# Kernel tuning notes

Hardware: AMD Instinct MI355X
Metric: run time of the kernel (lower is better)

Reference implementation:

```python
import jax, jax.numpy as jnp
import numpy as np
from jax import lax

B, S, V, U = 32, 512, 8000, 1024  # batch, seq_len, vocab, enc_units


def setup_inputs() -> dict:
    key = jax.random.key(0)
    ks = jax.random.split(key, 9)

    def p(k, shape, s=0.05):
        return jax.random.normal(k, shape, dtype=jnp.float32) * s

    inp = {"tokens": jax.random.randint(ks[0], (B, S), 0, V)}
    i = 1
    for d in ("f", "b"):  # forward / backward directions
        inp[f"W1{d}"] = p(ks[i], (V, 3 * U)); i += 1      # layer-1 input kernel (acts on one-hot)
        inp[f"R1{d}"] = p(ks[i], (U, 3 * U)); i += 1      # layer-1 recurrent kernel
        inp[f"b1{d}"] = jnp.zeros((2, 3 * U), jnp.float32)  # [input_bias, recurrent_bias] (reset_after)
        inp[f"W2{d}"] = p(ks[i], (U, 3 * U)); i += 1      # layer-2 input kernel
        inp[f"R2{d}"] = p(ks[i], (U, 3 * U)); i += 1
        inp[f"b2{d}"] = jnp.zeros((2, 3 * U), jnp.float32)
    return inp


def _gru_step(xz, h, R, rb):
    # Keras GRUCell, reset_after=True, inference (recurrent_dropout inactive).
    zi, ri, hi = jnp.split(xz, 3, axis=-1)
    rz, rr, rh = jnp.split(h @ R + rb, 3, axis=-1)
    z = jax.nn.sigmoid(zi + rz)
    r = jax.nn.sigmoid(ri + rr)
    hh = jnp.tanh(hi + r * rh)
    return z * h + (1.0 - z) * hh


def _run_dir(tokens, W1, R1, b1, W2, R2, b2, reverse):
    # one_hot(tokens) @ W1 == row gather of W1 (same math, no [B,S,V] one-hot materialized)
    x1 = jnp.take(W1, tokens, axis=0) + b1[0]  # [B, S, 3U]
    if reverse:
        x1 = x1[:, ::-1]
    units = R1.shape[0]
    h0 = jnp.zeros((tokens.shape[0], units), x1.dtype)

    def step(carry, xt):
        h1, h2 = carry
        h1 = _gru_step(xt, h1, R1, b1[1])
        h2 = _gru_step(h1 @ W2 + b2[0], h2, R2, b2[1])
        return (h1, h2), h2

    (h1, h2), ys = lax.scan(step, (h0, h0), jnp.swapaxes(x1, 0, 1))
    ys = jnp.swapaxes(ys, 0, 1)  # [B, S, U]
    if reverse:
        ys = ys[:, ::-1]
    return ys, h1, h2


def reference(tokens, W1f, R1f, b1f, W2f, R2f, b2f, W1b, R1b, b1b, W2b, R2b, b2b):
    yf, hf1, hf2 = _run_dir(tokens, W1f, R1f, b1f, W2f, R2f, b2f, False)
    yb, hb1, hb2 = _run_dir(tokens, W1b, R1b, b1b, W2b, R2b, b2b, True)
    output = jnp.concatenate([yf, yb], axis=-1)  # Bidirectional merge_mode='concat' -> [B,S,2U]
    # Faithful to the module's state indexing: s = [fwd_l1, fwd_l2, bwd_l1, bwd_l2];
    # getBidirectionalStates concatenates s[2i], s[2i+1].
    state1 = jnp.concatenate([hf1, hf2], axis=-1)
    state2 = jnp.concatenate([hb1, hb2], axis=-1)
    return output, state1, state2
```

## Files before the change

kernel.cpp:

```cpp
#include <hip/hip_runtime.h>
#include <stdint.h>

typedef __bf16 bf16x8 __attribute__((ext_vector_type(8)));
typedef float  f32x4  __attribute__((ext_vector_type(4)));

#define YSZ 33554432ull

#define R1L_OFF 0ull
#define R2L_OFF 12582912ull
#define W2L_OFF 25165824ull
#define HR1_OFF 37748736ull
#define HR2_OFF 39845888ull
#define X2R_OFF 41943040ull
#define FLG_OFF 48234496ull
#define WS_NEED 48238592ull

#define SM_RECW 0
#define SM_XW0  98304
#define SM_XW1  131072
#define SM_RED0 147456
#define SM_RED1 150528
#define SM_HST  153600
#define SM_XST  154624
#define SM_BYTES 156160

__device__ __forceinline__ unsigned short f2bf(float x){
  unsigned u; __builtin_memcpy(&u, &x, 4);
  u = (u + 0x7fffu + ((u >> 16) & 1u)) >> 16;
  return (unsigned short)u;
}
__device__ __forceinline__ float bf2f(unsigned short s){
  unsigned u = ((unsigned)s) << 16; float f; __builtin_memcpy(&f, &u, 4); return f;
}
__device__ __forceinline__ f32x4 mfma16(bf16x8 a, bf16x8 b, f32x4 c){
  return __builtin_amdgcn_mfma_f32_16x16x32_bf16(a, b, c, 0, 0, 0);
}

__global__ __launch_bounds__(256) void prep_weights(
    const float* __restrict__ R1f, const float* __restrict__ W2f, const float* __restrict__ R2f,
    const float* __restrict__ R1b, const float* __restrict__ W2b, const float* __restrict__ R2b,
    unsigned short* __restrict__ dst)
{
  unsigned c = blockIdx.x * 256u + threadIdx.x;
  if (c >= 2359296u) return;
  unsigned reg, cc;
  if (c < 786432u)       { reg = 0; cc = c; }
  else if (c < 1572864u) { reg = 1; cc = c - 786432u; }
  else                   { reg = 2; cc = c - 1572864u; }
  unsigned dirq = cc / 393216u; unsigned r = cc % 393216u;
  const float* src; unsigned col, ktbase, kg4;
  if (reg < 2) {
    unsigned a = r / 6144u; r %= 6144u;
    unsigned g = r / 2048u; r %= 2048u;
    unsigned kt = r >> 6;  unsigned l = r & 63u;
    col = g*1024u + a*16u + (l & 15u);
    ktbase = kt*32u; kg4 = (l >> 4)*4u;
    src = (reg==0) ? (dirq ? R1b : R1f) : (dirq ? R2b : R2f);
  } else {
    unsigned s = r / 3072u; unsigned rr = r % 3072u;
    unsigned c0 = s * 24u;
    if (rr < 2048u) { unsigned kt = rr >> 6, l = rr & 63u; col = c0 + (l & 15u); ktbase = kt*32u; kg4 = (l>>4)*4u; }
    else { unsigned q = rr - 2048u; unsigned kt = q >> 5, sl = q & 31u; col = c0 + 16u + (sl & 7u); ktbase = kt*32u; kg4 = (sl >> 3)*4u; }
    src = dirq ? W2b : W2f;
  }
  unsigned short* d = dst + (size_t)c * 8u;
  #pragma unroll
  for (int j = 0; j < 8; ++j) {
    unsigned k = ktbase + ((j >> 2) << 4) + kg4 + (j & 3);
    d[j] = f2bf(src[(size_t)k * 3072u + col]);
  }
}

__device__ __forceinline__ void poll_ge(unsigned* base, int lane, int tgt, long* budget){
  if (tgt <= 0 || *budget <= 0) return;
  long it = 0;
  while (1) {
    unsigned v = __hip_atomic_load(base + lane, __ATOMIC_RELAXED, __HIP_MEMORY_SCOPE_AGENT);
    if (__all((int)v >= tgt)) return;
    if (++it > *budget) { *budget = 0; return; }
    __builtin_amdgcn_s_sleep(1);
  }
}
__device__ __forceinline__ bf16x8 ld_frag(const char* slot, int kt, int mt, int lane){
  const uint64_t* p = (const uint64_t*)(slot + (((size_t)(kt*2 + mt)*64 + lane) << 4));
  union { uint64_t u[2]; bf16x8 v; } f;
  f.u[0] = __hip_atomic_load((uint64_t*)p,     __ATOMIC_RELAXED, __HIP_MEMORY_SCOPE_AGENT);
  f.u[1] = __hip_atomic_load((uint64_t*)p + 1, __ATOMIC_RELAXED, __HIP_MEMORY_SCOPE_AGENT);
  return f.v;
}
__device__ __forceinline__ void st16c(char* dst, const char* srcLDS){
  const uint64_t* s = (const uint64_t*)srcLDS;
  uint64_t a = s[0], b = s[1];
  __hip_atomic_store((uint64_t*)dst,     a, __ATOMIC_RELAXED, __HIP_MEMORY_SCOPE_AGENT);
  __hip_atomic_store((uint64_t*)dst + 1, b, __ATOMIC_RELAXED, __HIP_MEMORY_SCOPE_AGENT);
}

__global__ __launch_bounds__(256, 1) void enc_main(
    const int* __restrict__ tokens,
    const float* __restrict__ W1f, const float* __restrict__ W1b,
    const float* __restrict__ b1f, const float* __restrict__ b1b,
    const float* __restrict__ b2f, const float* __restrict__ b2b,
    char* __restrict__ ws, float* __restrict__ out)
{
  extern __shared__ char smem[];
  const int tid  = threadIdx.x;
  const int lane = tid & 63;
  const int wave = tid >> 6;
  const int mt   = wave >> 1;
  const int kh   = wave & 1;
  const int bid  = blockIdx.x;
  const int role = bid >> 6;
  const int idx  = bid & 63;
  const int dir  = role >> 1;
  const int isC  = role & 1;
  const int u0   = idx * 16;
  const int kt0  = u0 >> 5;
  const int uh8  = ((u0 >> 4) & 1) * 8;
  const int i16  = lane & 15;
  const int lg   = lane >> 4;

  {
    const size_t recoff = (isC ? R2L_OFF : R1L_OFF) + (size_t)(dir*64 + idx) * 98304;
    const uint4* rs = (const uint4*)(ws + recoff);
    uint4* rd = (uint4*)(smem + SM_RECW);
    #pragma unroll
    for (int i = 0; i < 24; ++i) rd[tid + 256*i] = rs[tid + 256*i];
    const size_t xoff = W2L_OFF + (size_t)(dir*128 + (isC ? 64 : 0) + idx) * 49152;
    const uint4* xs = (const uint4*)(ws + xoff);
    uint4* xd = (uint4*)(smem + SM_XW0);
    #pragma unroll
    for (int i = 0; i < 12; ++i) xd[tid + 256*i] = xs[tid + 256*i];
  }
  __syncthreads();

  unsigned* flags = (unsigned*)(ws + FLG_OFF);
  unsigned* fA1 = flags +   0 + dir*64;
  unsigned* fA2 = flags + 128 + dir*64;
  unsigned* fC1 = flags + 256 + dir*64;
  unsigned* fC2 = flags + 384 + dir*64;
  char* hr1 = ws + HR1_OFF + (size_t)dir * 16 * 65536;
  char* hr2 = ws + HR2_OFF + (size_t)dir * 16 * 65536;
  char* x2r = ws + X2R_OFF + (size_t)dir * 16 * 196608;
  const float* W1 = dir ? W1b : W1f;
  const float* b1 = dir ? b1b : b1f;
  const float* b2 = dir ? b2b : b2f;

  union FZ { uint64_t u[2]; bf16x8 v; };
  FZ fz; fz.u[0] = 0; fz.u[1] = 0;
  const bf16x8 zfrag = fz.v;

  long budget = 4000000;

  if (!isC) {
    const int c0x = idx * 24;
    bf16x8 hfr[16];
    #pragma unroll
    for (int q = 0; q < 16; ++q) hfr[q] = zfrag;
    float hold[4] = {0.f, 0.f, 0.f, 0.f};
    float x1z[4], x1r[4], x1h[4];
    float b0z=0,b0r=0,b0h=0,brz=0,brr=0,brh=0;
    if (kh == 0) {
      b0z = b1[u0 + i16]; b0r = b1[1024 + u0 + i16]; b0h = b1[2048 + u0 + i16];
      brz = b1[3072 + u0 + i16]; brr = b1[4096 + u0 + i16]; brh = b1[5120 + u0 + i16];
      int tt = dir ? 511 : 0;
      #pragma unroll
      for (int r = 0; r < 4; ++r) {
        int m = mt*16 + lg*4 + r;
        int tok = tokens[m*512 + tt];
        const float* p = W1 + (size_t)tok*3072 + u0 + i16;
        x1z[r] = p[0]; x1r[r] = p[1024]; x1h[r] = p[2048];
      }
    }
    for (int t = 0; t < 512; ++t) {
      float nz[4], nr[4], nh[4];
      if (kh == 0 && t < 511) {
        int tt = dir ? (510 - t) : (t + 1);
        #pragma unroll
        for (int r = 0; r < 4; ++r) {
          int m = mt*16 + lg*4 + r;
          int tok = tokens[m*512 + tt];
          const float* p = W1 + (size_t)tok*3072 + u0 + i16;
          nz[r] = p[0]; nr[r] = p[1024]; nh[r] = p[2048];
        }
      }
      f32x4 az = {0,0,0,0}, ar = {0,0,0,0}, ah = {0,0,0,0};
      #pragma unroll
      for (int q = 0; q < 16; ++q) {
        int kt = kh*16 + q;
        bf16x8 a = hfr[q];
        az = mfma16(a, *(const bf16x8*)(smem + SM_RECW +         (kt<<10) + (lane<<4)), az);
        ar = mfma16(a, *(const bf16x8*)(smem + SM_RECW + 32768 + (kt<<10) + (lane<<4)), ar);
        ah = mfma16(a, *(const bf16x8*)(smem + SM_RECW + 65536 + (kt<<10) + (lane<<4)), ah);
      }
      __syncthreads();
      if (kh == 1) {
        f32x4* red = (f32x4*)(smem + (mt ? SM_RED1 : SM_RED0));
        red[lane] = az; red[64 + lane] = ar; red[128 + lane] = ah;
      }
      __syncthreads();
      if (kh == 0) {
        const f32x4* red = (const f32x4*)(smem + (mt ? SM_RED1 : SM_RED0));
        f32x4 rz = red[lane], rr4 = red[64 + lane], rh = red[128 + lane];
        #pragma unroll
        for (int r = 0; r < 4; ++r) {
          float zp = x1z[r] + b0z + az[r] + rz[r] + brz;
          float rp = x1r[r] + b0r + ar[r] + rr4[r] + brr;
          float zg = 1.f / (1.f + __expf(-zp));
          float rg = 1.f / (1.f + __expf(-rp));
          float hp = (x1h[r] + b0h) + rg * (ah[r] + rh[r] + brh);
          float e2 = __expf(-2.f * hp);
          float th = (1.f - e2) / (1.f + e2);
          float hn = zg * hold[r] + (1.f - zg) * th;
          hold[r] = hn;
          *(unsigned short*)(smem + SM_HST + ((mt*16 + lg*4 + r)*16 + i16)*2) = f2bf(hn);
        }
        if (t == 511) {
          #pragma unroll
          for (int r = 0; r < 4; ++r)
            out[YSZ + (size_t)dir*65536 + (size_t)(mt*16 + lg*4 + r)*2048 + u0 + i16] = hold[r];
        }
      }
      __syncthreads();
      char* h1slot = hr1 + (size_t)(t & 15) * 65536;
      if (wave == 0) {
        poll_ge(fC1, lane, t - 15, &budget);
        #pragma unroll
        for (int mtl = 0; mtl < 2; ++mtl) {
          uint64_t v = *(const uint64_t*)(smem + SM_HST + (mtl*256 + (lane & 15)*16 + ((lane >> 4) << 2))*2);
          __hip_atomic_store((uint64_t*)(h1slot + (((size_t)(kt0*2 + mtl)*64 + lane) << 4) + uh8),
                             v, __ATOMIC_RELAXED, __HIP_MEMORY_SCOPE_AGENT);
        }
        if (lane == 0)
          __hip_atomic_store(fA1 + idx, (unsigned)(t + 1), __ATOMIC_RELEASE, __HIP_MEMORY_SCOPE_AGENT);
        poll_ge(fA1, lane, t + 1, &budget);
      }
      __syncthreads();
      #pragma unroll
      for (int q = 0; q < 16; ++q) hfr[q] = ld_frag(h1slot, kh*16 + q, mt, lane);
      f32x4 a0 = {0,0,0,0}, a1 = {0,0,0,0};
      #pragma unroll
      for (int q = 0; q < 16; ++q) {
        int kt = kh*16 + q;
        bf16x8 a = hfr[q];
        a0 = mfma16(a, *(const bf16x8*)(smem + SM_XW0 + (kt<<10) + (lane<<4)), a0);
        bf16x8 bb = zfrag;
        if (i16 < 8) bb = *(const bf16x8*)(smem + SM_XW1 + (kt<<9) + ((lg*8 + (lane & 7)) << 4));
        a1 = mfma16(a, bb, a1);
      }
      __syncthreads();
      if (kh == 1) {
        f32x4* red = (f32x4*)(smem + (mt ? SM_RED1 : SM_RED0));
        red[lane] = a0; red[64 + lane] = a1;
      }
      __syncthreads();
      if (kh == 0) {
        const f32x4* red = (const f32x4*)(smem + (mt ? SM_RED1 : SM_RED0));
        f32x4 r0 = red[lane], r1 = red[64 + lane];
        #pragma unroll
        for (int r = 0; r < 4; ++r) {
          int m = mt*16 + lg*4 + r;
          *(unsigned short*)(smem + SM_XST + (i16*32 + m)*2) = f2bf(a0[r] + r0[r]);
          if (i16 < 8)
            *(unsigned short*)(smem + SM_XST + ((16 + i16)*32 + m)*2) = f2bf(a1[r] + r1[r]);
        }
      }
      __syncthreads();
      if (wave == 0) {
        char* xslot = x2r + (size_t)(t & 15) * 196608;
        st16c(xslot + (size_t)(c0x + (lane >> 2))*64 + (lane & 3)*16,
              smem + SM_XST + (lane >> 2)*64 + (lane & 3)*16);
        if (lane < 32) {
          int c = 64 + lane;
          st16c(xslot + (size_t)(c0x + (c >> 2))*64 + (c & 3)*16,
                smem + SM_XST + (c >> 2)*64 + (c & 3)*16);
        }
        if (lane == 0)
          __hip_atomic_store(fA2 + idx, (unsigned)(t + 1), __ATOMIC_RELEASE, __HIP_MEMORY_SCOPE_AGENT);
      }
      if (kh == 0 && t < 511) {
        #pragma unroll
        for (int r = 0; r < 4; ++r) { x1z[r] = nz[r]; x1r[r] = nr[r]; x1h[r] = nh[r]; }
      }
    }
  } else {
    const int c0x = 1536 + idx * 24;
    bf16x8 hf2[16], hf1[16];
    #pragma unroll
    for (int q = 0; q < 16; ++q) { hf2[q] = zfrag; hf1[q] = zfrag; }
    float hold[4] = {0.f, 0.f, 0.f, 0.f};
    float b0z=0,b0r=0,b0h=0,brz=0,brr=0,brh=0;
    if (kh == 0) {
      b0z = b2[u0 + i16]; b0r = b2[1024 + u0 + i16]; b0h = b2[2048 + u0 + i16];
      brz = b2[3072 + u0 + i16]; brr = b2[4096 + u0 + i16]; brh = b2[5120 + u0 + i16];
    }
    for (int t = 0; t < 512; ++t) {
      if (wave == 0 && t > 0) poll_ge(fC1, lane, t, &budget);
      __syncthreads();
      if (t > 0) {
        char* h2slot = hr2 + (size_t)((t - 1) & 15) * 65536;
        #pragma unroll
        for (int q = 0; q < 16; ++q) hf2[q] = ld_frag(h2slot, kh*16 + q, mt, lane);
      }
      f32x4 az = {0,0,0,0}, ar = {0,0,0,0}, ah = {0,0,0,0};
      #pragma unroll
      for (int q = 0; q < 16; ++q) {
        int kt = kh*16 + q;
        bf16x8 a = hf2[q];
        az = mfma16(a, *(const bf16x8*)(smem + SM_RECW +         (kt<<10) + (lane<<4)), az);
        ar = mfma16(a, *(const bf16x8*)(smem + SM_RECW + 32768 + (kt<<10) + (lane<<4)), ar);
        ah = mfma16(a, *(const bf16x8*)(smem + SM_RECW + 65536 + (kt<<10) + (lane<<4)), ah);
      }
      __syncthreads();
      if (kh == 1) {
        f32x4* red = (f32x4*)(smem + (mt ? SM_RED1 : SM_RED0));
        red[lane] = az; red[64 + lane] = ar; red[128 + lane] = ah;
      }
      __syncthreads();
      f32x4 rz = {0,0,0,0}, rr4 = {0,0,0,0}, rh = {0,0,0,0};
      if (kh == 0) {
        const f32x4* red = (const f32x4*)(smem + (mt ? SM_RED1 : SM_RED0));
        rz = red[lane]; rr4 = red[64 + lane]; rh = red[128 + lane];
      }
      if (wave == 0) poll_ge(fA1, lane, t + 1, &budget);
      __syncthreads();
      char* h1slot = hr1 + (size_t)(t & 15) * 65536;
      #pragma unroll
      for (int q = 0; q < 16; ++q) hf1[q] = ld_frag(h1slot, kh*16 + q, mt, lane);
      f32x4 a0 = {0,0,0,0}, a1 = {0,0,0,0};
      #pragma unroll
      for (int q = 0; q < 16; ++q) {
        int kt = kh*16 + q;
        bf16x8 a = hf1[q];
        a0 = mfma16(a, *(const bf16x8*)(smem + SM_XW0 + (kt<<10) + (lane<<4)), a0);
        bf16x8 bb = zfrag;
        if (i16 < 8) bb = *(const bf16x8*)(smem + SM_XW1 + (kt<<9) + ((lg*8 + (lane & 7)) << 4));
        a1 = mfma16(a, bb, a1);
      }
      __syncthreads();
      if (kh == 1) {
        f32x4* red = (f32x4*)(smem + (mt ? SM_RED1 : SM_RED0));
        red[lane] = a0; red[64 + lane] = a1;
      }
      __syncthreads();
      if (kh == 0) {
        const f32x4* red = (const f32x4*)(smem + (mt ? SM_RED1 : SM_RED0));
        f32x4 r0 = red[lane], r1 = red[64 + lane];
        #pragma unroll
        for (int r = 0; r < 4; ++r) {
          int m = mt*16 + lg*4 + r;
          *(unsigned short*)(smem + SM_XST + (i16*32 + m)*2) = f2bf(a0[r] + r0[r]);
          if (i16 < 8)
            *(unsigned short*)(smem + SM_XST + ((16 + i16)*32 + m)*2) = f2bf(a1[r] + r1[r]);
        }
      }
      __syncthreads();
      char* xslot = x2r + (size_t)(t & 15) * 196608;
      if (wave == 0) {
        st16c(xslot + (size_t)(c0x + (lane >> 2))*64 + (lane & 3)*16,
              smem + SM_XST + (lane >> 2)*64 + (lane & 3)*16);
        if (lane < 32) {
          int c = 64 + lane;
          st16c(xslot + (size_t)(c0x + (c >> 2))*64 + (c & 3)*16,
                smem + SM_XST + (c >> 2)*64 + (c & 3)*16);
        }
        if (lane == 0)
          __hip_atomic_store(fC2 + idx, (unsigned)(t + 1), __ATOMIC_RELEASE, __HIP_MEMORY_SCOPE_AGENT);
        poll_ge(fA2, lane, t + 1, &budget);
        poll_ge(fC2, lane, t + 1, &budget);
      }
      __syncthreads();
      if (kh == 0) {
        int m0 = mt*16 + lg*4;
        float xg[3][4];
        #pragma unroll
        for (int g = 0; g < 3; ++g) {
          uint64_t v = __hip_atomic_load(
              (uint64_t*)(xslot + ((size_t)(g*1024 + u0 + i16)*32 + m0)*2),
              __ATOMIC_RELAXED, __HIP_MEMORY_SCOPE_AGENT);
          #pragma unroll
          for (int r = 0; r < 4; ++r) xg[g][r] = bf2f((unsigned short)(v >> (16*r)));
        }
        int tt = dir ? (511 - t) : t;
        #pragma unroll
        for (int r = 0; r < 4; ++r) {
          float zp = xg[0][r] + b0z + az[r] + rz[r] + brz;
          float rp = xg[1][r] + b0r + ar[r] + rr4[r] + brr;
          float zg = 1.f / (1.f + __expf(-zp));
          float rg = 1.f / (1.f + __expf(-rp));
          float hp = (xg[2][r] + b0h) + rg * (ah[r] + rh[r] + brh);
          float e2 = __expf(-2.f * hp);
          float th = (1.f - e2) / (1.f + e2);
          float hn = zg * hold[r] + (1.f - zg) * th;
          hold[r] = hn;
          *(unsigned short*)(smem + SM_HST + ((mt*16 + lg*4 + r)*16 + i16)*2) = f2bf(hn);
          int m = m0 + r;
          out[((size_t)m*512 + tt)*2048 + dir*1024 + u0 + i16] = hn;
          if (t == 511)
            out[YSZ + (size_t)dir*65536 + (size_t)m*2048 + 1024 + u0 + i16] = hn;
        }
      }
      __syncthreads();
      if (wave == 0) {
        char* h2slot = hr2 + (size_t)(t & 15) * 65536;
        #pragma unroll
        for (int mtl = 0; mtl < 2; ++mtl) {
          uint64_t v = *(const uint64_t*)(smem + SM_HST + (mtl*256 + (lane & 15)*16 + ((lane >> 4) << 2))*2);
          __hip_atomic_store((uint64_t*)(h2slot + (((size_t)(kt0*2 + mtl)*64 + lane) << 4) + uh8),
                             v, __ATOMIC_RELAXED, __HIP_MEMORY_SCOPE_AGENT);
        }
        if (lane == 0)
          __hip_atomic_store(fC1 + idx, (unsigned)(t + 1), __ATOMIC_RELEASE, __HIP_MEMORY_SCOPE_AGENT);
      }
    }
  }
}

extern "C" void kernel_launch(void* const* d_in, const int* in_sizes, int n_in,
                              void* d_out, int out_size, void* d_ws, size_t ws_size,
                              hipStream_t stream)
{
  const int*   tokens = (const int*)d_in[0];
  const float* W1f = (const float*)d_in[1];
  const float* R1f = (const float*)d_in[2];
  const float* b1f = (const float*)d_in[3];
  const float* W2f = (const float*)d_in[4];
  const float* R2f = (const float*)d_in[5];
  const float* b2f = (const float*)d_in[6];
  const float* W1b = (const float*)d_in[7];
  const float* R1b = (const float*)d_in[8];
  const float* b1b = (const float*)d_in[9];
  const float* W2b = (const float*)d_in[10];
  const float* R2b = (const float*)d_in[11];
  const float* b2b = (const float*)d_in[12];
  char* ws = (char*)d_ws;
  (void)in_sizes; (void)n_in; (void)out_size;
  if (ws_size < WS_NEED) return;

  hipMemsetAsync(ws + FLG_OFF, 0, 4096, stream);
  prep_weights<<<9216, 256, 0, stream>>>(R1f, W2f, R2f, R1b, W2b, R2b, (unsigned short*)ws);
  hipFuncSetAttribute((const void*)enc_main, hipFuncAttributeMaxDynamicSharedMemorySize, 163840);
  enc_main<<<256, 256, SM_BYTES, stream>>>(tokens, W1f, W1b, b1f, b1b, b2f, b2b, ws, (float*)d_out);
}
```

Before: 10.14 ms.

## Move layer-2 input projection into layer-2 blocks and drop x2 exchange buffer

```diff
diff --git a/kernel.cpp b/kernel.cpp
--- a/kernel.cpp
+++ b/kernel.cpp
@@ -11,58 +11,45 @@
 #define W2L_OFF 25165824ull
 #define HR1_OFF 37748736ull
 #define HR2_OFF 39845888ull
-#define X2R_OFF 41943040ull
-#define FLG_OFF 48234496ull
-#define WS_NEED 48238592ull
+#define FLG_OFF 41943040ull
+#define WS_NEED 41947136ull
 
 #define SM_RECW 0
-#define SM_XW0  98304
-#define SM_XW1  131072
-#define SM_RED0 147456
-#define SM_RED1 150528
-#define SM_HST  153600
-#define SM_XST  154624
-#define SM_BYTES 156160
+#define SM_XWH  98304
+#define SM_RED0 131072
+#define SM_RED1 135168
+#define SM_HST  139264
+#define SM_BYTES 140288
 
 __device__ __forceinline__ unsigned short f2bf(float x){
   unsigned u; __builtin_memcpy(&u, &x, 4);
   u = (u + 0x7fffu + ((u >> 16) & 1u)) >> 16;
   return (unsigned short)u;
 }
-__device__ __forceinline__ float bf2f(unsigned short s){
-  unsigned u = ((unsigned)s) << 16; float f; __builtin_memcpy(&f, &u, 4); return f;
-}
 __device__ __forceinline__ f32x4 mfma16(bf16x8 a, bf16x8 b, f32x4 c){
   return __builtin_amdgcn_mfma_f32_16x16x32_bf16(a, b, c, 0, 0, 0);
 }
 
 __global__ __launch_bounds__(256) void prep_weights(
-    const float* __restrict__ R1f, const float* __restrict__ W2f, const float* __restrict__ R2f,
-    const float* __restrict__ R1b, const float* __restrict__ W2b, const float* __restrict__ R2b,
+    const float* __restrict__ R1f, const float* __restrict__ R2f, const float* __restrict__ W2f,
+    const float* __restrict__ R1b, const float* __restrict__ R2b, const float* __restrict__ W2b,
     unsigned short* __restrict__ dst)
 {
   unsigned c = blockIdx.x * 256u + threadIdx.x;
   if (c >= 2359296u) return;
-  unsigned reg, cc;
-  if (c < 786432u)       { reg = 0; cc = c; }
-  else if (c < 1572864u) { reg = 1; cc = c - 786432u; }
-  else                   { reg = 2; cc = c - 1572864u; }
-  unsigned dirq = cc / 393216u; unsigned r = cc % 393216u;
-  const float* src; unsigned col, ktbase, kg4;
-  if (reg < 2) {
-    unsigned a = r / 6144u; r %= 6144u;
-    unsigned g = r / 2048u; r %= 2048u;
-    unsigned kt = r >> 6;  unsigned l = r & 63u;
-    col = g*1024u + a*16u + (l & 15u);
-    ktbase = kt*32u; kg4 = (l >> 4)*4u;
-    src = (reg==0) ? (dirq ? R1b : R1f) : (dirq ? R2b : R2f);
-  } else {
-    unsigned s = r / 3072u; unsigned rr = r % 3072u;
-    unsigned c0 = s * 24u;
-    if (rr < 2048u) { unsigned kt = rr >> 6, l = rr & 63u; col = c0 + (l & 15u); ktbase = kt*32u; kg4 = (l>>4)*4u; }
-    else { unsigned q = rr - 2048u; unsigned kt = q >> 5, sl = q & 31u; col = c0 + 16u + (sl & 7u); ktbase = kt*32u; kg4 = (sl >> 3)*4u; }
-    src = dirq ? W2b : W2f;
-  }
+  unsigned reg = c / 786432u;
+  unsigned cc  = c % 786432u;
+  unsigned dirq = cc / 393216u;
+  unsigned r = cc % 393216u;
+  unsigned a = r / 6144u; r %= 6144u;
+  unsigned g = r / 2048u; r %= 2048u;
+  unsigned kt = r >> 6; unsigned l = r & 63u;
+  unsigned col = g*1024u + a*16u + (l & 15u);
+  unsigned ktbase = kt*32u, kg4 = (l >> 4)*4u;
+  const float* src;
+  if (reg == 0)      src = dirq ? R1b : R1f;
+  else if (reg == 1) src = dirq ? R2b : R2f;
+  else               src = dirq ? W2b : W2f;
   unsigned short* d = dst + (size_t)c * 8u;
   #pragma unroll
   for (int j = 0; j < 8; ++j) {
@@ -71,11 +58,13 @@
   }
 }
 
-__device__ __forceinline__ void poll_ge(unsigned* base, int lane, int tgt, long* budget){
+__device__ __forceinline__ void poll_ge2(unsigned* base, int lane, int tgt, long* budget){
   if (tgt <= 0 || *budget <= 0) return;
   long it = 0;
   while (1) {
-    unsigned v = __hip_atomic_load(base + lane, __ATOMIC_RELAXED, __HIP_MEMORY_SCOPE_AGENT);
+    unsigned v0 = __hip_atomic_load(base + lane,      __ATOMIC_RELAXED, __HIP_MEMORY_SCOPE_AGENT);
+    unsigned v1 = __hip_atomic_load(base + 64 + lane, __ATOMIC_RELAXED, __HIP_MEMORY_SCOPE_AGENT);
+    unsigned v = v0 < v1 ? v0 : v1;
     if (__all((int)v >= tgt)) return;
     if (++it > *budget) { *budget = 0; return; }
     __builtin_amdgcn_s_sleep(1);
@@ -88,11 +77,11 @@
   f.u[1] = __hip_atomic_load((uint64_t*)p + 1, __ATOMIC_RELAXED, __HIP_MEMORY_SCOPE_AGENT);
   return f.v;
 }
-__device__ __forceinline__ void st16c(char* dst, const char* srcLDS){
-  const uint64_t* s = (const uint64_t*)srcLDS;
-  uint64_t a = s[0], b = s[1];
-  __hip_atomic_store((uint64_t*)dst,     a, __ATOMIC_RELAXED, __HIP_MEMORY_SCOPE_AGENT);
-  __hip_atomic_store((uint64_t*)dst + 1, b, __ATOMIC_RELAXED, __HIP_MEMORY_SCOPE_AGENT);
+__device__ __forceinline__ uint64_t lds_transpose_read(const char* p){
+  asm volatile("" ::: "memory");
+  __builtin_amdgcn_sched_barrier(0);
+  uint64_t v; __builtin_memcpy(&v, p, 8);
+  return v;
 }
 
 __global__ __launch_bounds__(256, 1) void enc_main(
@@ -119,44 +108,35 @@
   const int i16  = lane & 15;
   const int lg   = lane >> 4;
 
+  unsigned* flags = (unsigned*)(ws + FLG_OFF);
+  unsigned* fA1 = flags + dir*128;
+  unsigned* fC1 = flags + 256 + dir*128;
+  char* hr1 = ws + HR1_OFF + (size_t)dir * 1048576;
+  char* hr2 = ws + HR2_OFF + (size_t)dir * 1048576;
+  const float* b1 = dir ? b1b : b1f;
+  const float* b2 = dir ? b2b : b2f;
+  const float* W1 = dir ? W1b : W1f;
+
+  union FZ { uint64_t u[2]; bf16x8 v; };
+  FZ fz; fz.u[0] = 0; fz.u[1] = 0;
+  const bf16x8 zfrag = fz.v;
+
+  long budget = 2000000;
+
   {
     const size_t recoff = (isC ? R2L_OFF : R1L_OFF) + (size_t)(dir*64 + idx) * 98304;
     const uint4* rs = (const uint4*)(ws + recoff);
     uint4* rd = (uint4*)(smem + SM_RECW);
     #pragma unroll
     for (int i = 0; i < 24; ++i) rd[tid + 256*i] = rs[tid + 256*i];
-    const size_t xoff = W2L_OFF + (size_t)(dir*128 + (isC ? 64 : 0) + idx) * 49152;
-    const uint4* xs = (const uint4*)(ws + xoff);
-    uint4* xd = (uint4*)(smem + SM_XW0);
-    #pragma unroll
-    for (int i = 0; i < 12; ++i) xd[tid + 256*i] = xs[tid + 256*i];
   }
-  __syncthreads();
-
-  unsigned* flags = (unsigned*)(ws + FLG_OFF);
-  unsigned* fA1 = flags +   0 + dir*64;
-  unsigned* fA2 = flags + 128 + dir*64;
-  unsigned* fC1 = flags + 256 + dir*64;
-  unsigned* fC2 = flags + 384 + dir*64;
-  char* hr1 = ws + HR1_OFF + (size_t)dir * 16 * 65536;
-  char* hr2 = ws + HR2_OFF + (size_t)dir * 16 * 65536;
-  char* x2r = ws + X2R_OFF + (size_t)dir * 16 * 196608;
-  const float* W1 = dir ? W1b : W1f;
-  const float* b1 = dir ? b1b : b1f;
-  const float* b2 = dir ? b2b : b2f;
-
-  union FZ { uint64_t u[2]; bf16x8 v; };
-  FZ fz; fz.u[0] = 0; fz.u[1] = 0;
-  const bf16x8 zfrag = fz.v;
-
-  long budget = 4000000;
 
   if (!isC) {
-    const int c0x = idx * 24;
+    __syncthreads();
     bf16x8 hfr[16];
     #pragma unroll
     for (int q = 0; q < 16; ++q) hfr[q] = zfrag;
-    float hold[4] = {0.f, 0.f, 0.f, 0.f};
+    float hold[4] = {0.f,0.f,0.f,0.f};
     float x1z[4], x1r[4], x1h[4];
     float b0z=0,b0r=0,b0h=0,brz=0,brr=0,brh=0;
     if (kh == 0) {
@@ -198,6 +178,7 @@
         red[lane] = az; red[64 + lane] = ar; red[128 + lane] = ah;
       }
       __syncthreads();
+      char* h1slot = hr1 + (size_t)(t & 15) * 65536;
       if (kh == 0) {
         const f32x4* red = (const f32x4*)(smem + (mt ? SM_RED1 : SM_RED0));
         f32x4 rz = red[lane], rr4 = red[64 + lane], rh = red[128 + lane];
@@ -214,202 +195,112 @@
           hold[r] = hn;
           *(unsigned short*)(smem + SM_HST + ((mt*16 + lg*4 + r)*16 + i16)*2) = f2bf(hn);
         }
-        if (t == 511) {
+        uint64_t v = lds_transpose_read(smem + SM_HST + ((mt*16 + i16)*16 + lg*4)*2);
+        if ((t & 7) == 0) poll_ge2(fC1, lane, t - 7, &budget);
+        __hip_atomic_store((uint64_t*)(h1slot + (((size_t)(kt0*2 + mt)*64 + lane) << 4) + uh8),
+                           v, __ATOMIC_RELAXED, __HIP_MEMORY_SCOPE_AGENT);
+        if (lane == 0)
+          __hip_atomic_store(fA1 + mt*64 + idx, (unsigned)(t + 1), __ATOMIC_RELEASE, __HIP_MEMORY_SCOPE_AGENT);
+      }
+      if (t < 511) {
+        poll_ge2(fA1, lane, t + 1, &budget);
+        #pragma unroll
+        for (int q = 0; q < 16; ++q) hfr[q] = ld_frag(h1slot, kh*16 + q, mt, lane);
+        if (kh == 0) {
           #pragma unroll
-          for (int r = 0; r < 4; ++r)
-            out[YSZ + (size_t)dir*65536 + (size_t)(mt*16 + lg*4 + r)*2048 + u0 + i16] = hold[r];
-        }
-      }
-      __syncthreads();
-      char* h1slot = hr1 + (size_t)(t & 15) * 65536;
-      if (wave == 0) {
-        poll_ge(fC1, lane, t - 15, &budget);
-        #pragma unroll
-        for (int mtl = 0; mtl < 2; ++mtl) {
-          uint64_t v = *(const uint64_t*)(smem + SM_HST + (mtl*256 + (lane & 15)*16 + ((lane >> 4) << 2))*2);
-          __hip_atomic_store((uint64_t*)(h1slot + (((size_t)(kt0*2 + mtl)*64 + lane) << 4) + uh8),
-                             v, __ATOMIC_RELAXED, __HIP_MEMORY_SCOPE_AGENT);
-        }
-        if (lane == 0)
-          __hip_atomic_store(fA1 + idx, (unsigned)(t + 1), __ATOMIC_RELEASE, __HIP_MEMORY_SCOPE_AGENT);
-        poll_ge(fA1, lane, t + 1, &budget);
-      }
-      __syncthreads();
-      #pragma unroll
-      for (int q = 0; q < 16; ++q) hfr[q] = ld_frag(h1slot, kh*16 + q, mt, lane);
-      f32x4 a0 = {0,0,0,0}, a1 = {0,0,0,0};
+          for (int r = 0; r < 4; ++r) { x1z[r] = nz[r]; x1r[r] = nr[r]; x1h[r] = nh[r]; }
+        }
+      } else if (kh == 0) {
+        #pragma unroll
+        for (int r = 0; r < 4; ++r)
+          out[YSZ + (size_t)dir*65536 + (size_t)(mt*16 + lg*4 + r)*2048 + u0 + i16] = hold[r];
+      }
+    }
+  } else {
+    bf16x8 w2z[16], w2r[16];
+    {
+      const size_t w2off = W2L_OFF + (size_t)(dir*64 + idx) * 98304;
+      const uint4* xs = (const uint4*)(ws + w2off + 65536);
+      uint4* xd = (uint4*)(smem + SM_XWH);
+      #pragma unroll
+      for (int i = 0; i < 8; ++i) xd[tid + 256*i] = xs[tid + 256*i];
+      const char* wb = ws + w2off;
       #pragma unroll
       for (int q = 0; q < 16; ++q) {
         int kt = kh*16 + q;
-        bf16x8 a = hfr[q];
-        a0 = mfma16(a, *(const bf16x8*)(smem + SM_XW0 + (kt<<10) + (lane<<4)), a0);
-        bf16x8 bb = zfrag;
-        if (i16 < 8) bb = *(const bf16x8*)(smem + SM_XW1 + (kt<<9) + ((lg*8 + (lane & 7)) << 4));
-        a1 = mfma16(a, bb, a1);
-      }
-      __syncthreads();
-      if (kh == 1) {
-        f32x4* red = (f32x4*)(smem + (mt ? SM_RED1 : SM_RED0));
-        red[lane] = a0; red[64 + lane] = a1;
-      }
-      __syncthreads();
-      if (kh == 0) {
-        const f32x4* red = (const f32x4*)(smem + (mt ? SM_RED1 : SM_RED0));
-        f32x4 r0 = red[lane], r1 = red[64 + lane];
-        #pragma unroll
-        for (int r = 0; r < 4; ++r) {
-          int m = mt*16 + lg*4 + r;
-          *(unsigned short*)(smem + SM_XST + (i16*32 + m)*2) = f2bf(a0[r] + r0[r]);
-          if (i16 < 8)
-            *(unsigned short*)(smem + SM_XST + ((16 + i16)*32 + m)*2) = f2bf(a1[r] + r1[r]);
-        }
-      }
-      __syncthreads();
-      if (wave == 0) {
-        char* xslot = x2r + (size_t)(t & 15) * 196608;
-        st16c(xslot + (size_t)(c0x + (lane >> 2))*64 + (lane & 3)*16,
-              smem + SM_XST + (lane >> 2)*64 + (lane & 3)*16);
-        if (lane < 32) {
-          int c = 64 + lane;
-          st16c(xslot + (size_t)(c0x + (c >> 2))*64 + (c & 3)*16,
-                smem + SM_XST + (c >> 2)*64 + (c & 3)*16);
-        }
-        if (lane == 0)
-          __hip_atomic_store(fA2 + idx, (unsigned)(t + 1), __ATOMIC_RELEASE, __HIP_MEMORY_SCOPE_AGENT);
-      }
-      if (kh == 0 && t < 511) {
-        #pragma unroll
-        for (int r = 0; r < 4; ++r) { x1z[r] = nz[r]; x1r[r] = nr[r]; x1h[r] = nh[r]; }
-      }
-    }
-  } else {
-    const int c0x = 1536 + idx * 24;
-    bf16x8 hf2[16], hf1[16];
-    #pragma unroll
-    for (int q = 0; q < 16; ++q) { hf2[q] = zfrag; hf1[q] = zfrag; }
-    float hold[4] = {0.f, 0.f, 0.f, 0.f};
+        w2z[q] = *(const bf16x8*)(wb +          ((size_t)(kt*64 + lane) << 4));
+        w2r[q] = *(const bf16x8*)(wb + 32768 + ((size_t)(kt*64 + lane) << 4));
+      }
+    }
+    __syncthreads();
+    float hold[4] = {0.f,0.f,0.f,0.f};
     float b0z=0,b0r=0,b0h=0,brz=0,brr=0,brh=0;
     if (kh == 0) {
       b0z = b2[u0 + i16]; b0r = b2[1024 + u0 + i16]; b0h = b2[2048 + u0 + i16];
       brz = b2[3072 + u0 + i16]; brr = b2[4096 + u0 + i16]; brh = b2[5120 + u0 + i16];
     }
     for (int t = 0; t < 512; ++t) {
-      if (wave == 0 && t > 0) poll_ge(fC1, lane, t, &budget);
-      __syncthreads();
-      if (t > 0) {
-        char* h2slot = hr2 + (size_t)((t - 1) & 15) * 65536;
-        #pragma unroll
-        for (int q = 0; q < 16; ++q) hf2[q] = ld_frag(h2slot, kh*16 + q, mt, lane);
-      }
-      f32x4 az = {0,0,0,0}, ar = {0,0,0,0}, ah = {0,0,0,0};
+      poll_ge2(fA1, lane, t + 1, &budget);
+      char* h1slot = hr1 + (size_t)(t & 15) * 65536;
+      f32x4 xz = {0,0,0,0}, xr = {0,0,0,0}, xh = {0,0,0,0};
       #pragma unroll
       for (int q = 0; q < 16; ++q) {
         int kt = kh*16 + q;
-        bf16x8 a = hf2[q];
-        az = mfma16(a, *(const bf16x8*)(smem + SM_RECW +         (kt<<10) + (lane<<4)), az);
-        ar = mfma16(a, *(const bf16x8*)(smem + SM_RECW + 32768 + (kt<<10) + (lane<<4)), ar);
-        ah = mfma16(a, *(const bf16x8*)(smem + SM_RECW + 65536 + (kt<<10) + (lane<<4)), ah);
-      }
+        bf16x8 a = ld_frag(h1slot, kt, mt, lane);
+        xz = mfma16(a, w2z[q], xz);
+        xr = mfma16(a, w2r[q], xr);
+        xh = mfma16(a, *(const bf16x8*)(smem + SM_XWH + (kt<<10) + (lane<<4)), xh);
+      }
+      f32x4 az = {0,0,0,0}, ar = {0,0,0,0}, ah = {0,0,0,0};
+      if (t > 0) {
+        poll_ge2(fC1, lane, t, &budget);
+        char* h2slot = hr2 + (size_t)((t - 1) & 15) * 65536;
+        #pragma unroll
+        for (int q = 0; q < 16; ++q) {
+          int kt = kh*16 + q;
+          bf16x8 a = ld_frag(h2slot, kt, mt, lane);
+          az = mfma16(a, *(const bf16x8*)(smem + SM_RECW +         (kt<<10) + (lane<<4)), az);
+          ar = mfma16(a, *(const bf16x8*)(smem + SM_RECW + 32768 + (kt<<10) + (lane<<4)), ar);
+          ah = mfma16(a, *(const bf16x8*)(smem + SM_RECW + 65536 + (kt<<10) + (lane<<4)), ah);
+        }
+      }
+      az += xz; ar += xr;
       __syncthreads();
       if (kh == 1) {
         f32x4* red = (f32x4*)(smem + (mt ? SM_RED1 : SM_RED0));
-        red[lane] = az; red[64 + lane] = ar; red[128 + lane] = ah;
-      }
-      __syncthreads();
-      f32x4 rz = {0,0,0,0}, rr4 = {0,0,0,0}, rh = {0,0,0,0};
-      if (kh == 0) {
-        const f32x4* red = (const f32x4*)(smem + (mt ? SM_RED1 : SM_RED0));
-        rz = red[lane]; rr4 = red[64 + lane]; rh = red[128 + lane];
-      }
-      if (wave == 0) poll_ge(fA1, lane, t + 1, &budget);
-      __syncthreads();
-      char* h1slot = hr1 + (size_t)(t & 15) * 65536;
-      #pragma unroll
-      for (int q = 0; q < 16; ++q) hf1[q] = ld_frag(h1slot, kh*16 + q, mt, lane);
-      f32x4 a0 = {0,0,0,0}, a1 = {0,0,0,0};
-      #pragma unroll
-      for (int q = 0; q < 16; ++q) {
-        int kt = kh*16 + q;
-        bf16x8 a = hf1[q];
-        a0 = mfma16(a, *(const bf16x8*)(smem + SM_XW0 + (kt<<10) + (lane<<4)), a0);
-        bf16x8 bb = zfrag;
-        if (i16 < 8) bb = *(const bf16x8*)(smem + SM_XW1 + (kt<<9) + ((lg*8 + (lane & 7)) << 4));
-        a1 = mfma16(a, bb, a1);
-      }
-      __syncthreads();
-      if (kh == 1) {
-        f32x4* red = (f32x4*)(smem + (mt ? SM_RED1 : SM_RED0));
-        red[lane] = a0; red[64 + lane] = a1;
+        red[lane] = az; red[64 + lane] = ar; red[128 + lane] = ah; red[192 + lane] = xh;
       }
       __syncthreads();
       if (kh == 0) {
         const f32x4* red = (const f32x4*)(smem + (mt ? SM_RED1 : SM_RED0));
-        f32x4 r0 = red[lane], r1 = red[64 + lane];
+        f32x4 rz = red[lane], rr4 = red[64 + lane], rh = red[128 + lane], rxh = red[192 + lane];
         #pragma unroll
         for (int r = 0; r < 4; ++r) {
-          int m = mt*16 + lg*4 + r;
-          *(unsigned short*)(smem + SM_XST + (i16*32 + m)*2) = f2bf(a0[r] + r0[r]);
-          if (i16 < 8)
-            *(unsigned short*)(smem + SM_XST + ((16 + i16)*32 + m)*2) = f2bf(a1[r] + r1[r]);
-        }
-      }
-      __syncthreads();
-      char* xslot = x2r + (size_t)(t & 15) * 196608;
-      if (wave == 0) {
-        st16c(xslot + (size_t)(c0x + (lane >> 2))*64 + (lane & 3)*16,
-              smem + SM_XST + (lane >> 2)*64 + (lane & 3)*16);
-        if (lane < 32) {
-          int c = 64 + lane;
-          st16c(xslot + (size_t)(c0x + (c >> 2))*64 + (c & 3)*16,
-                smem + SM_XST + (c >> 2)*64 + (c & 3)*16);
-        }
-        if (lane == 0)
-          __hip_atomic_store(fC2 + idx, (unsigned)(t + 1), __ATOMIC_RELEASE, __HIP_MEMORY_SCOPE_AGENT);
-        poll_ge(fA2, lane, t + 1, &budget);
-        poll_ge(fC2, lane, t + 1, &budget);
-      }
-      __syncthreads();
-      if (kh == 0) {
-        int m0 = mt*16 + lg*4;
-        float xg[3][4];
-        #pragma unroll
-        for (int g = 0; g < 3; ++g) {
-          uint64_t v = __hip_atomic_load(
-              (uint64_t*)(xslot + ((size_t)(g*1024 + u0 + i16)*32 + m0)*2),
-              __ATOMIC_RELAXED, __HIP_MEMORY_SCOPE_AGENT);
-          #pragma unroll
-          for (int r = 0; r < 4; ++r) xg[g][r] = bf2f((unsigned short)(v >> (16*r)));
-        }
-        int tt = dir ? (511 - t) : t;
-        #pragma unroll
-        for (int r = 0; r < 4; ++r) {
-          float zp = xg[0][r] + b0z + az[r] + rz[r] + brz;
-          float rp = xg[1][r] + b0r + ar[r] + rr4[r] + brr;
+          float zp = az[r] + rz[r] + b0z + brz;
+          float rp = ar[r] + rr4[r] + b0r + brr;
           float zg = 1.f / (1.f + __expf(-zp));
           float rg = 1.f / (1.f + __expf(-rp));
-          float hp = (xg[2][r] + b0h) + rg * (ah[r] + rh[r] + brh);
+          float hp = (xh[r] + rxh[r] + b0h) + rg * (ah[r] + rh[r] + brh);
           float e2 = __expf(-2.f * hp);
           float th = (1.f - e2) / (1.f + e2);
           float hn = zg * hold[r] + (1.f - zg) * th;
           hold[r] = hn;
           *(unsigned short*)(smem + SM_HST + ((mt*16 + lg*4 + r)*16 + i16)*2) = f2bf(hn);
-          int m = m0 + r;
-          out[((size_t)m*512 + tt)*2048 + dir*1024 + u0 + i16] = hn;
+        }
+        char* h2slot = hr2 + (size_t)(t & 15) * 65536;
+        uint64_t v = lds_transpose_read(smem + SM_HST + ((mt*16 + i16)*16 + lg*4)*2);
+        __hip_atomic_store((uint64_t*)(h2slot + (((size_t)(kt0*2 + mt)*64 + lane) << 4) + uh8),
+                           v, __ATOMIC_RELAXED, __HIP_MEMORY_SCOPE_AGENT);
+        if (lane == 0)
+          __hip_atomic_store(fC1 + mt*64 + idx, (unsigned)(t + 1), __ATOMIC_RELEASE, __HIP_MEMORY_SCOPE_AGENT);
+        int tt = dir ? (511 - t) : t;
+        #pragma unroll
+        for (int r = 0; r < 4; ++r) {
+          int m = mt*16 + lg*4 + r;
+          out[((size_t)m*512 + tt)*2048 + dir*1024 + u0 + i16] = hold[r];
           if (t == 511)
-            out[YSZ + (size_t)dir*65536 + (size_t)m*2048 + 1024 + u0 + i16] = hn;
-        }
-      }
-      __syncthreads();
-      if (wave == 0) {
-        char* h2slot = hr2 + (size_t)(t & 15) * 65536;
-        #pragma unroll
-        for (int mtl = 0; mtl < 2; ++mtl) {
-          uint64_t v = *(const uint64_t*)(smem + SM_HST + (mtl*256 + (lane & 15)*16 + ((lane >> 4) << 2))*2);
-          __hip_atomic_store((uint64_t*)(h2slot + (((size_t)(kt0*2 + mtl)*64 + lane) << 4) + uh8),
-                             v, __ATOMIC_RELAXED, __HIP_MEMORY_SCOPE_AGENT);
-        }
-        if (lane == 0)
-          __hip_atomic_store(fC1 + idx, (unsigned)(t + 1), __ATOMIC_RELEASE, __HIP_MEMORY_SCOPE_AGENT);
+            out[YSZ + (size_t)dir*65536 + (size_t)m*2048 + 1024 + u0 + i16] = hold[r];
+        }
       }
     }
   }
@@ -437,7 +328,7 @@
   if (ws_size < WS_NEED) return;
 
   hipMemsetAsync(ws + FLG_OFF, 0, 4096, stream);
-  prep_weights<<<9216, 256, 0, stream>>>(R1f, W2f, R2f, R1b, W2b, R2b, (unsigned short*)ws);
+  prep_weights<<<9216, 256, 0, stream>>>(R1f, R2f, W2f, R1b, R2b, W2b, (unsigned short*)ws);
   hipFuncSetAttribute((const void*)enc_main, hipFuncAttributeMaxDynamicSharedMemorySize, 163840);
   enc_main<<<256, 256, SM_BYTES, stream>>>(tokens, W1f, W1b, b1f, b1b, b2f, b2b, ws, (float*)d_out);
 }
```

After: 10.45 ms. 3.1% more time.
